# Kernel tuning notes

Measured on AMD Instinct MI355X. Metric: run time of the kernel, lower is better.

## Reference

```python
import math
import jax, jax.numpy as jnp
import numpy as np

B, S, D, N, H = 4, 1024, 1024, 16, 64

def setup_inputs() -> dict:
    key = jax.random.key(0)
    ks = jax.random.split(key, 10)
    sc = 0.02
    return {
        'from_tensor': jax.random.normal(ks[0], (B, S, D), jnp.float32),
        'to_tensor': jax.random.normal(ks[1], (B, S, D), jnp.float32),
        'attention_mask': jnp.ones((B, S, S), jnp.int32),
        'wq': jax.random.normal(ks[2], (D, N, H), jnp.float32) * sc,
        'bq': jnp.zeros((N, H), jnp.float32),
        'wk': jax.random.normal(ks[3], (D, N, H), jnp.float32) * sc,
        'bk': jnp.zeros((N, H), jnp.float32),
        'wv': jax.random.normal(ks[4], (D, N, H), jnp.float32) * sc,
        'bv': jnp.zeros((N, H), jnp.float32),
        'pre_softmax_weight': jax.random.normal(ks[5], (N, N), jnp.float32) * sc,
        'post_softmax_weight': jax.random.normal(ks[6], (N, N), jnp.float32) * sc,
        'wo': jax.random.normal(ks[7], (N, H, D), jnp.float32) * sc,
        'bo': jnp.zeros((D,), jnp.float32),
    }

def reference(from_tensor, to_tensor, attention_mask, wq, bq, wk, bk, wv, bv,
              pre_softmax_weight, post_softmax_weight, wo, bo):
    # QKV projections: [B,S,D] x [D,N,H] -> [B,S,N,H]
    q = jnp.einsum('bfd,dnh->bfnh', from_tensor, wq) + bq
    k = jnp.einsum('btd,dnh->btnh', to_tensor, wk) + bk
    v = jnp.einsum('btd,dnh->btnh', to_tensor, wv) + bv
    # attention scores [B,N,F,T]
    scores = jnp.einsum('btnh,bfnh->bnft', k, q) * (1.0 / math.sqrt(float(H)))
    # pre-softmax head mixing
    scores = jnp.einsum('bnft,nl->blft', scores, pre_softmax_weight)
    # masked softmax (mask expanded at axis 1, additive -10000 on masked)
    mask = attention_mask.astype(scores.dtype)[:, None, :, :]  # [B,1,F,T]
    scores = scores + (1.0 - mask) * -10000.0
    probs = jax.nn.softmax(scores, axis=-1)
    # post-softmax head mixing (dropout rate 0.0 -> identity)
    probs = jnp.einsum('bnft,nl->blft', probs, post_softmax_weight)
    # attend to values and project out
    ctx = jnp.einsum('bnft,btnh->bfnh', probs, v)
    out = jnp.einsum('bfnh,nhd->bfd', ctx, wo) + bo
    return out
```

## Files before the change

kernel.cpp:

```cpp
#include <hip/hip_runtime.h>
#include <hip/hip_bf16.h>

typedef __hip_bfloat16 bf16;
using short8 = __attribute__((ext_vector_type(8))) short;
using f32x4  = __attribute__((ext_vector_type(4))) float;
using f32x2  = __attribute__((ext_vector_type(2))) float;

#ifndef __has_builtin
#define __has_builtin(x) 0
#endif
#if __has_builtin(__builtin_amdgcn_global_load_lds)
#define HAVE_GLL 1
#else
#define HAVE_GLL 0
#endif

__device__ inline void stage16(const short* __restrict__ g, short* l, int lane) {
#if HAVE_GLL
  __builtin_amdgcn_global_load_lds((__attribute__((address_space(1))) void*)g,
                                   (__attribute__((address_space(3))) void*)l,
                                   16, 0, 0);
#else
  *(short8*)(l + lane * 8) = *(const short8*)g;
#endif
}

__device__ inline unsigned pack2bf(float a, float b) {
  bf16 h0 = __float2bfloat16(a), h1 = __float2bfloat16(b);
  return (unsigned)*(unsigned short*)&h0 | ((unsigned)*(unsigned short*)&h1 << 16);
}

__global__ __launch_bounds__(256) void gemm_lds64(
    const bf16* __restrict__ Ag, long a_bs1, long a_bs2, int lda,
    const bf16* __restrict__ Bg, long b_bs1, long b_bs2, int ldb,
    void* __restrict__ Cg, long c_bs1, long c_bs2, int ldc,
    const float* __restrict__ bias, int K, int Z2, float alpha, int cf32)
{
  __shared__ short As[128 * 64];
  __shared__ short Bs[64 * 64];

  int z = blockIdx.z, z1 = z / Z2, z2 = z - z1 * Z2;
  const short* A = (const short*)(Ag + z1 * a_bs1 + z2 * a_bs2);
  const short* B = (const short*)(Bg + z1 * b_bs1 + z2 * b_bs2);

  int tid = threadIdx.x, lane = tid & 63, w = tid >> 6;
  int wm = w & 1, wn = w >> 1;
  int m0 = blockIdx.x * 128, n0 = blockIdx.y * 64;
  int r = lane & 15, q = lane >> 4;

  int srow = lane >> 3, scol = (lane & 7) * 8;
  const short* Asrc = A + (long)(m0 + w * 32 + srow) * lda + scol;
  const short* Bsrc = B + (long)(n0 + w * 16 + srow) * ldb + scol;
  short* Adst = As + (w * 32) * 64;
  short* Bdst = Bs + (w * 16) * 64;

  f32x4 acc[4][2];
  #pragma unroll
  for (int i = 0; i < 4; ++i)
    #pragma unroll
    for (int j = 0; j < 2; ++j) acc[i][j] = (f32x4){0.f, 0.f, 0.f, 0.f};

  for (int kt = 0; kt < K; kt += 64) {
    #pragma unroll
    for (int i = 0; i < 4; ++i)
      stage16(Asrc + (long)i * 8 * lda + kt, Adst + i * 8 * 64, lane);
    #pragma unroll
    for (int i = 0; i < 2; ++i)
      stage16(Bsrc + (long)i * 8 * ldb + kt, Bdst + i * 8 * 64, lane);
    __syncthreads();
    #pragma unroll
    for (int kk = 0; kk < 64; kk += 32) {
      short8 af[4], bfr[2];
      #pragma unroll
      for (int i = 0; i < 4; ++i)
        af[i] = *(const short8*)&As[(wm * 64 + i * 16 + r) * 64 + kk + q * 8];
      #pragma unroll
      for (int j = 0; j < 2; ++j)
        bfr[j] = *(const short8*)&Bs[(wn * 32 + j * 16 + r) * 64 + kk + q * 8];
      #pragma unroll
      for (int i = 0; i < 4; ++i)
        #pragma unroll
        for (int j = 0; j < 2; ++j)
          acc[i][j] = __builtin_amdgcn_mfma_f32_16x16x32_bf16(af[i], bfr[j], acc[i][j], 0, 0, 0);
    }
    __syncthreads();
  }

  long cb = z1 * c_bs1 + z2 * c_bs2;
  #pragma unroll
  for (int j = 0; j < 2; ++j) {
    int col = n0 + wn * 32 + j * 16 + r;
    float bv = bias ? bias[col] : 0.0f;
    #pragma unroll
    for (int i = 0; i < 4; ++i) {
      int row0 = m0 + wm * 64 + i * 16 + q * 4;
      #pragma unroll
      for (int rr = 0; rr < 4; ++rr) {
        float val = acc[i][j][rr] * alpha + bv;
        long idx = cb + (long)(row0 + rr) * ldc + col;
        if (cf32) ((float*)Cg)[idx] = val;
        else ((bf16*)Cg)[idx] = __float2bfloat16(val);
      }
    }
  }
}

struct QKVArgs {
  const bf16* A[3];
  const bf16* Bw[3];
  bf16* C[3];
  const float* bias[3];
};

__global__ __launch_bounds__(256) void gemm_qkv(QKVArgs args) {
  __shared__ short As[128 * 64];
  __shared__ short Bs[64 * 64];

  int z = blockIdx.z;
  const short* A = (const short*)args.A[z];
  const short* B = (const short*)args.Bw[z];
  bf16* C = args.C[z];
  const float* bias = args.bias[z];

  int tid = threadIdx.x, lane = tid & 63, w = tid >> 6;
  int wm = w & 1, wn = w >> 1;
  int m0 = blockIdx.x * 128, n0 = blockIdx.y * 64;
  int r = lane & 15, q = lane >> 4;

  int srow = lane >> 3, scol = (lane & 7) * 8;
  const short* Asrc = A + (long)(m0 + w * 32 + srow) * 1024 + scol;
  const short* Bsrc = B + (long)(n0 + w * 16 + srow) * 1024 + scol;
  short* Adst = As + (w * 32) * 64;
  short* Bdst = Bs + (w * 16) * 64;

  f32x4 acc[4][2];
  #pragma unroll
  for (int i = 0; i < 4; ++i)
    #pragma unroll
    for (int j = 0; j < 2; ++j) acc[i][j] = (f32x4){0.f, 0.f, 0.f, 0.f};

  for (int kt = 0; kt < 1024; kt += 64) {
    #pragma unroll
    for (int i = 0; i < 4; ++i)
      stage16(Asrc + (long)i * 8 * 1024 + kt, Adst + i * 8 * 64, lane);
    #pragma unroll
    for (int i = 0; i < 2; ++i)
      stage16(Bsrc + (long)i * 8 * 1024 + kt, Bdst + i * 8 * 64, lane);
    __syncthreads();
    #pragma unroll
    for (int kk = 0; kk < 64; kk += 32) {
      short8 af[4], bfr[2];
      #pragma unroll
      for (int i = 0; i < 4; ++i)
        af[i] = *(const short8*)&As[(wm * 64 + i * 16 + r) * 64 + kk + q * 8];
      #pragma unroll
      for (int j = 0; j < 2; ++j)
        bfr[j] = *(const short8*)&Bs[(wn * 32 + j * 16 + r) * 64 + kk + q * 8];
      #pragma unroll
      for (int i = 0; i < 4; ++i)
        #pragma unroll
        for (int j = 0; j < 2; ++j)
          acc[i][j] = __builtin_amdgcn_mfma_f32_16x16x32_bf16(af[i], bfr[j], acc[i][j], 0, 0, 0);
    }
    __syncthreads();
  }

  #pragma unroll
  for (int j = 0; j < 2; ++j) {
    int col = n0 + wn * 32 + j * 16 + r;
    float bv = bias[col];
    #pragma unroll
    for (int i = 0; i < 4; ++i) {
      int row0 = m0 + wm * 64 + i * 16 + q * 4;
      #pragma unroll
      for (int rr = 0; rr < 4; ++rr)
        C[(long)(row0 + rr) * 1024 + col] = __float2bfloat16(acc[i][j][rr] + bv);
    }
  }
}

__global__ __launch_bounds__(256) void gemm_k64(
    const bf16* __restrict__ Ag, long a_bs1, long a_bs2, int lda,
    const bf16* __restrict__ Bg, long b_bs1, long b_bs2, int ldb,
    bf16* __restrict__ Cg, long c_bs1, long c_bs2, int ldc,
    int Z2, float alpha)
{
  int z = blockIdx.z, z1 = z / Z2, z2 = z - z1 * Z2;
  const short* A = (const short*)(Ag + z1 * a_bs1 + z2 * a_bs2);
  const short* B = (const short*)(Bg + z1 * b_bs1 + z2 * b_bs2);
  bf16* C = Cg + z1 * c_bs1 + z2 * c_bs2;

  int tid = threadIdx.x, lane = tid & 63, w = tid >> 6;
  int wm = w & 1, wn = w >> 1;
  int m0 = blockIdx.x * 128 + wm * 64;
  int n0 = blockIdx.y * 128 + wn * 64;
  int r = lane & 15, q = lane >> 4;

  const short* Ar = A + (long)(m0 + r) * lda + q * 8;
  const short* Br = B + (long)(n0 + r) * ldb + q * 8;

  f32x4 acc[4][4];
  #pragma unroll
  for (int i = 0; i < 4; ++i)
    #pragma unroll
    for (int j = 0; j < 4; ++j) acc[i][j] = (f32x4){0.f, 0.f, 0.f, 0.f};

  #pragma unroll
  for (int kk = 0; kk < 64; kk += 32) {
    short8 af[4], bfr[4];
    #pragma unroll
    for (int i = 0; i < 4; ++i) af[i] = *(const short8*)(Ar + (long)i * 16 * lda + kk);
    #pragma unroll
    for (int j = 0; j < 4; ++j) bfr[j] = *(const short8*)(Br + (long)j * 16 * ldb + kk);
    #pragma unroll
    for (int i = 0; i < 4; ++i)
      #pragma unroll
      for (int j = 0; j < 4; ++j)
        acc[i][j] = __builtin_amdgcn_mfma_f32_16x16x32_bf16(af[i], bfr[j], acc[i][j], 0, 0, 0);
  }

  #pragma unroll
  for (int j = 0; j < 4; ++j) {
    int col = n0 + j * 16 + r;
    #pragma unroll
    for (int i = 0; i < 4; ++i) {
      int row0 = m0 + i * 16 + q * 4;
      #pragma unroll
      for (int rr = 0; rr < 4; ++rr)
        C[(long)(row0 + rr) * ldc + col] = __float2bfloat16(acc[i][j][rr] * alpha);
    }
  }
}

__global__ __launch_bounds__(256) void cvt2(
    const float* __restrict__ a, const float* __restrict__ b,
    bf16* __restrict__ oa, bf16* __restrict__ ob)
{
  const float* in = blockIdx.y ? b : a;
  bf16* out = blockIdx.y ? ob : oa;
  int i = (blockIdx.x * 256 + threadIdx.x) * 8;
  float4 v0 = *(const float4*)(in + i);
  float4 v1 = *(const float4*)(in + i + 4);
  uint4 pk;
  pk.x = pack2bf(v0.x, v0.y);
  pk.y = pack2bf(v0.z, v0.w);
  pk.z = pack2bf(v1.x, v1.y);
  pk.w = pack2bf(v1.z, v1.w);
  *(uint4*)(out + i) = pk;
}

struct WT4 { const float* s[4]; bf16* d[4]; };

__global__ __launch_bounds__(256) void wtrans4(WT4 a) {
  __shared__ bf16 tile[64][66];
  int z = blockIdx.z;
  const float* in = a.s[z];
  bf16* out = a.d[z];
  int r0 = blockIdx.x * 64, c0 = blockIdx.y * 64;
  int tx = threadIdx.x & 63, ty = threadIdx.x >> 6;
  #pragma unroll
  for (int i = 0; i < 16; ++i) {
    int rr = i * 4 + ty;
    tile[rr][tx] = __float2bfloat16(in[(long)(r0 + rr) * 1024 + c0 + tx]);
  }
  __syncthreads();
  #pragma unroll
  for (int i = 0; i < 16; ++i) {
    int rr = i * 4 + ty;
    out[(long)(c0 + rr) * 1024 + r0 + tx] = tile[tx][rr];
  }
}

__global__ __launch_bounds__(256) void transpose_bf16(
    const bf16* __restrict__ in, long i_bs1, long i_bs2, int i_rs,
    bf16* __restrict__ out, long o_bs1, long o_bs2, int o_rs, int Z2)
{
  __shared__ bf16 tile[64][66];
  int z = blockIdx.z, z1 = z / Z2, z2 = z - z1 * Z2;
  const bf16* ib = in + z1 * i_bs1 + z2 * i_bs2;
  bf16* ob = out + z1 * o_bs1 + z2 * o_bs2;
  int r0 = blockIdx.x * 64, c0 = blockIdx.y * 64;
  int tx = threadIdx.x & 63, ty = threadIdx.x >> 6;
  #pragma unroll
  for (int i = 0; i < 16; ++i) {
    int rr = i * 4 + ty;
    tile[rr][tx] = ib[(long)(r0 + rr) * i_rs + c0 + tx];
  }
  __syncthreads();
  #pragma unroll
  for (int i = 0; i < 16; ++i) {
    int rr = i * 4 + ty;
    ob[(long)(c0 + rr) * o_rs + r0 + tx] = tile[tx][rr];
  }
}

__global__ __launch_bounds__(256) void mixsoftmax2(
    bf16* __restrict__ sc, long sc_bs, const float* __restrict__ pre,
    const float* __restrict__ post, const int* __restrict__ mask)
{
  __shared__ float wpre[256], wpost[256];
  __shared__ float zbuf[16][256];
  __shared__ float zbuf2[16][16];
  __shared__ float zinv[16];
  int tid = threadIdx.x;
  int f = blockIdx.x, b = blockIdx.y;
  wpre[tid] = pre[tid];
  wpost[tid] = post[tid];
  __syncthreads();

  unsigned short* scb = (unsigned short*)(sc + (long)b * sc_bs) + ((long)f << 10);
  const int* mk = mask + ((long)b << 20) + ((long)f << 10);
  int tg = tid * 4;

  uint2 u[16];
  #pragma unroll
  for (int n = 0; n < 16; ++n)
    u[n] = *(const uint2*)(scb + ((long)n << 20) + tg);
  int4 mm = *(const int4*)(mk + tg);
  float madd0 = (1.0f - (float)mm.x) * -10000.0f;
  float madd1 = (1.0f - (float)mm.y) * -10000.0f;
  float madd2 = (1.0f - (float)mm.z) * -10000.0f;
  float madd3 = (1.0f - (float)mm.w) * -10000.0f;

  f32x2 mA[16], mB[16];
  #pragma unroll
  for (int l = 0; l < 16; ++l) {
    mA[l] = (f32x2){madd0, madd1};
    mB[l] = (f32x2){madd2, madd3};
  }

  #pragma unroll
  for (int n = 0; n < 16; ++n) {
    unsigned lo = u[n].x, hi = u[n].y;
    f32x2 s01 = (f32x2){__uint_as_float((lo & 0xffffu) << 16),
                        __uint_as_float(lo & 0xffff0000u)};
    f32x2 s23 = (f32x2){__uint_as_float((hi & 0xffffu) << 16),
                        __uint_as_float(hi & 0xffff0000u)};
    const float4* wr = (const float4*)&wpre[n * 16];
    #pragma unroll
    for (int g = 0; g < 4; ++g) {
      float4 wv = wr[g];
      mA[g * 4 + 0] += s01 * wv.x;  mB[g * 4 + 0] += s23 * wv.x;
      mA[g * 4 + 1] += s01 * wv.y;  mB[g * 4 + 1] += s23 * wv.y;
      mA[g * 4 + 2] += s01 * wv.z;  mB[g * 4 + 2] += s23 * wv.z;
      mA[g * 4 + 3] += s01 * wv.w;  mB[g * 4 + 3] += s23 * wv.w;
    }
  }

  #pragma unroll
  for (int l = 0; l < 16; ++l) {
    mA[l].x = __expf(mA[l].x);  mA[l].y = __expf(mA[l].y);
    mB[l].x = __expf(mB[l].x);  mB[l].y = __expf(mB[l].y);
    zbuf[l][tid] = (mA[l].x + mA[l].y) + (mB[l].x + mB[l].y);
  }
  __syncthreads();
  {
    int l = tid >> 4, c = tid & 15;
    const float4* zr = (const float4*)&zbuf[l][c * 16];
    float4 a0 = zr[0], a1 = zr[1], a2 = zr[2], a3 = zr[3];
    zbuf2[l][c] = ((a0.x + a0.y) + (a0.z + a0.w)) + ((a1.x + a1.y) + (a1.z + a1.w)) +
                  ((a2.x + a2.y) + (a2.z + a2.w)) + ((a3.x + a3.y) + (a3.z + a3.w));
  }
  __syncthreads();
  if (tid < 16) {
    const float4* zr = (const float4*)&zbuf2[tid][0];
    float4 a0 = zr[0], a1 = zr[1], a2 = zr[2], a3 = zr[3];
    float s = ((a0.x + a0.y) + (a0.z + a0.w)) + ((a1.x + a1.y) + (a1.z + a1.w)) +
              ((a2.x + a2.y) + (a2.z + a2.w)) + ((a3.x + a3.y) + (a3.z + a3.w));
    zinv[tid] = 1.0f / s;
  }
  __syncthreads();

  f32x2 oA[16], oB[16];
  #pragma unroll
  for (int l = 0; l < 16; ++l) {
    oA[l] = (f32x2){0.f, 0.f};
    oB[l] = (f32x2){0.f, 0.f};
  }
  #pragma unroll
  for (int n = 0; n < 16; ++n) {
    float zi = zinv[n];
    f32x2 e01 = mA[n] * zi, e23 = mB[n] * zi;
    const float4* wr = (const float4*)&wpost[n * 16];
    #pragma unroll
    for (int g = 0; g < 4; ++g) {
      float4 wv = wr[g];
      oA[g * 4 + 0] += e01 * wv.x;  oB[g * 4 + 0] += e23 * wv.x;
      oA[g * 4 + 1] += e01 * wv.y;  oB[g * 4 + 1] += e23 * wv.y;
      oA[g * 4 + 2] += e01 * wv.z;  oB[g * 4 + 2] += e23 * wv.z;
      oA[g * 4 + 3] += e01 * wv.w;  oB[g * 4 + 3] += e23 * wv.w;
    }
  }
  #pragma unroll
  for (int l = 0; l < 16; ++l) {
    uint2 st;
    st.x = pack2bf(oA[l].x, oA[l].y);
    st.y = pack2bf(oB[l].x, oB[l].y);
    *(uint2*)(scb + ((long)l << 20) + tg) = st;
  }
}

extern "C" void kernel_launch(void* const* d_in, const int* in_sizes, int n_in,
                              void* d_out, int out_size, void* d_ws, size_t ws_size,
                              hipStream_t stream) {
  const float* from = (const float*)d_in[0];
  const float* to   = (const float*)d_in[1];
  const int*  mask  = (const int*)d_in[2];
  const float* wq = (const float*)d_in[3];
  const float* bq = (const float*)d_in[4];
  const float* wk = (const float*)d_in[5];
  const float* bk = (const float*)d_in[6];
  const float* wv = (const float*)d_in[7];
  const float* bv = (const float*)d_in[8];
  const float* pre  = (const float*)d_in[9];
  const float* post = (const float*)d_in[10];
  const float* wo = (const float*)d_in[11];
  const float* bo = (const float*)d_in[12];
  float* out = (float*)d_out;

  bf16* W = (bf16*)d_ws;
  const long M1 = 1048576;
  bool big = ws_size >= (size_t)(85 * M1) * 2;

  bf16 *Sc, *fromB, *toB, *wqT, *wkT, *wvT, *woT, *Q, *Kp, *V, *Vt, *ctx;
  if (big) {
    Sc = W;                 fromB = W;            toB = W + 4 * M1;
    wqT = W + 8 * M1;       wkT = W + 9 * M1;     wvT = W + 10 * M1;
    woT = W + 64 * M1;      Q = W + 65 * M1;      Kp = W + 69 * M1;
    V = W + 73 * M1;        Vt = W + 77 * M1;     ctx = W + 81 * M1;
  } else {
    Sc = W;                 fromB = W;            toB = W + 4 * M1;
    wqT = W + 8 * M1;       wkT = W + 9 * M1;     wvT = W + 10 * M1;
    woT = W + 16 * M1;      Q = W + 17 * M1;      Kp = W + 21 * M1;
    V = W + 25 * M1;        Vt = W + 29 * M1;     ctx = W + 33 * M1;
  }

  dim3 blk(256);

  cvt2<<<dim3(2048, 2), blk, 0, stream>>>(from, to, fromB, toB);
  WT4 wt;
  wt.s[0] = wq; wt.s[1] = wk; wt.s[2] = wv; wt.s[3] = wo;
  wt.d[0] = wqT; wt.d[1] = wkT; wt.d[2] = wvT; wt.d[3] = woT;
  wtrans4<<<dim3(16, 16, 4), blk, 0, stream>>>(wt);

  QKVArgs qa;
  qa.A[0] = fromB; qa.A[1] = toB; qa.A[2] = toB;
  qa.Bw[0] = wqT;  qa.Bw[1] = wkT; qa.Bw[2] = wvT;
  qa.C[0] = Q;     qa.C[1] = Kp;  qa.C[2] = V;
  qa.bias[0] = bq; qa.bias[1] = bk; qa.bias[2] = bv;
  gemm_qkv<<<dim3(32, 16, 3), blk, 0, stream>>>(qa);

  transpose_bf16<<<dim3(16, 1, 64), blk, 0, stream>>>(V, M1, 64, 1024,
                                                      Vt, M1, 65536, 1024, 16);

  if (big) {
    gemm_k64<<<dim3(8, 8, 64), blk, 0, stream>>>(
        Q, M1, 64, 1024, Kp, M1, 64, 1024, Sc, 16 * M1, M1, 1024, 16, 0.125f);
    mixsoftmax2<<<dim3(1024, 4), blk, 0, stream>>>(Sc, 16 * M1, pre, post, mask);
    gemm_lds64<<<dim3(8, 1, 64), blk, 0, stream>>>(
        Sc, 16 * M1, M1, 1024, Vt, M1, 65536, 1024, ctx, M1, 64, 1024, nullptr,
        1024, 16, 1.0f, 0);
  } else {
    for (int b = 0; b < 4; ++b) {
      gemm_k64<<<dim3(8, 8, 16), blk, 0, stream>>>(
          Q + b * M1, 0, 64, 1024, Kp + b * M1, 0, 64, 1024,
          Sc, 0, M1, 1024, 16, 0.125f);
      mixsoftmax2<<<dim3(1024, 1), blk, 0, stream>>>(Sc, 0, pre, post, mask + b * M1);
      gemm_lds64<<<dim3(8, 1, 16), blk, 0, stream>>>(
          Sc, 0, M1, 1024, Vt + b * M1, 0, 65536, 1024,
          ctx + b * M1, 0, 64, 1024, nullptr, 1024, 16, 1.0f, 0);
    }
  }

  gemm_lds64<<<dim3(32, 16, 1), blk, 0, stream>>>(
      ctx, 0, 0, 1024, woT, 0, 0, 1024, out, 0, 0, 1024, bo, 1024, 1, 1.0f, 1);
}
```

Measured before the change: 347.3 us.

## Use MFMA for softmax head mixing and widen projection GEMM N-tiles

Rewrites the mix-softmax kernel so that the pre- and post-softmax 16x16 head-mixing matmuls run on bf16 MFMA instructions instead of scalar FMAs. Scores are staged through padded LDS and row sums are reduced with wave shuffles. Separately, the QKV and output projection GEMMs move from 64- to 128-wide N tiles, halving their grid and increasing reuse of each A tile. Running the head mixing in bf16 MFMA rounds the mixing weights and the probabilities to bf16, which costs some precision. The larger tiles raise register and LDS use per block.

```diff
diff --git a/kernel.cpp b/kernel.cpp
--- a/kernel.cpp
+++ b/kernel.cpp
@@ -4,7 +4,6 @@
 typedef __hip_bfloat16 bf16;
 using short8 = __attribute__((ext_vector_type(8))) short;
 using f32x4  = __attribute__((ext_vector_type(4))) float;
-using f32x2  = __attribute__((ext_vector_type(2))) float;
 
 #ifndef __has_builtin
 #define __has_builtin(x) 0
@@ -30,14 +29,21 @@
   return (unsigned)*(unsigned short*)&h0 | ((unsigned)*(unsigned short*)&h1 << 16);
 }
 
-__global__ __launch_bounds__(256) void gemm_lds64(
+__device__ inline short bfbits(float v) {
+  bf16 h = __float2bfloat16(v);
+  return *(short*)&h;
+}
+
+template <int BN>
+__global__ __launch_bounds__(256) void gemm_lds(
     const bf16* __restrict__ Ag, long a_bs1, long a_bs2, int lda,
     const bf16* __restrict__ Bg, long b_bs1, long b_bs2, int ldb,
     void* __restrict__ Cg, long c_bs1, long c_bs2, int ldc,
     const float* __restrict__ bias, int K, int Z2, float alpha, int cf32)
 {
+  constexpr int WNT = BN / 32;
   __shared__ short As[128 * 64];
-  __shared__ short Bs[64 * 64];
+  __shared__ short Bs[BN * 64];
 
   int z = blockIdx.z, z1 = z / Z2, z2 = z - z1 * Z2;
   const short* A = (const short*)(Ag + z1 * a_bs1 + z2 * a_bs2);
@@ -45,42 +51,42 @@
 
   int tid = threadIdx.x, lane = tid & 63, w = tid >> 6;
   int wm = w & 1, wn = w >> 1;
-  int m0 = blockIdx.x * 128, n0 = blockIdx.y * 64;
+  int m0 = blockIdx.x * 128, n0 = blockIdx.y * BN;
   int r = lane & 15, q = lane >> 4;
 
   int srow = lane >> 3, scol = (lane & 7) * 8;
   const short* Asrc = A + (long)(m0 + w * 32 + srow) * lda + scol;
-  const short* Bsrc = B + (long)(n0 + w * 16 + srow) * ldb + scol;
+  const short* Bsrc = B + (long)(n0 + w * (BN / 4) + srow) * ldb + scol;
   short* Adst = As + (w * 32) * 64;
-  short* Bdst = Bs + (w * 16) * 64;
-
-  f32x4 acc[4][2];
+  short* Bdst = Bs + (w * (BN / 4)) * 64;
+
+  f32x4 acc[4][WNT];
   #pragma unroll
   for (int i = 0; i < 4; ++i)
     #pragma unroll
-    for (int j = 0; j < 2; ++j) acc[i][j] = (f32x4){0.f, 0.f, 0.f, 0.f};
+    for (int j = 0; j < WNT; ++j) acc[i][j] = (f32x4){0.f, 0.f, 0.f, 0.f};
 
   for (int kt = 0; kt < K; kt += 64) {
     #pragma unroll
     for (int i = 0; i < 4; ++i)
       stage16(Asrc + (long)i * 8 * lda + kt, Adst + i * 8 * 64, lane);
     #pragma unroll
-    for (int i = 0; i < 2; ++i)
+    for (int i = 0; i < BN / 32; ++i)
       stage16(Bsrc + (long)i * 8 * ldb + kt, Bdst + i * 8 * 64, lane);
     __syncthreads();
     #pragma unroll
     for (int kk = 0; kk < 64; kk += 32) {
-      short8 af[4], bfr[2];
+      short8 af[4], bfr[WNT];
       #pragma unroll
       for (int i = 0; i < 4; ++i)
         af[i] = *(const short8*)&As[(wm * 64 + i * 16 + r) * 64 + kk + q * 8];
       #pragma unroll
-      for (int j = 0; j < 2; ++j)
-        bfr[j] = *(const short8*)&Bs[(wn * 32 + j * 16 + r) * 64 + kk + q * 8];
+      for (int j = 0; j < WNT; ++j)
+        bfr[j] = *(const short8*)&Bs[(wn * WNT * 16 + j * 16 + r) * 64 + kk + q * 8];
       #pragma unroll
       for (int i = 0; i < 4; ++i)
         #pragma unroll
-        for (int j = 0; j < 2; ++j)
+        for (int j = 0; j < WNT; ++j)
           acc[i][j] = __builtin_amdgcn_mfma_f32_16x16x32_bf16(af[i], bfr[j], acc[i][j], 0, 0, 0);
     }
     __syncthreads();
@@ -88,8 +94,8 @@
 
   long cb = z1 * c_bs1 + z2 * c_bs2;
   #pragma unroll
-  for (int j = 0; j < 2; ++j) {
-    int col = n0 + wn * 32 + j * 16 + r;
+  for (int j = 0; j < WNT; ++j) {
+    int col = n0 + wn * WNT * 16 + j * 16 + r;
     float bv = bias ? bias[col] : 0.0f;
     #pragma unroll
     for (int i = 0; i < 4; ++i) {
@@ -114,7 +120,7 @@
 
 __global__ __launch_bounds__(256) void gemm_qkv(QKVArgs args) {
   __shared__ short As[128 * 64];
-  __shared__ short Bs[64 * 64];
+  __shared__ short Bs[128 * 64];
 
   int z = blockIdx.z;
   const short* A = (const short*)args.A[z];
@@ -124,50 +130,50 @@
 
   int tid = threadIdx.x, lane = tid & 63, w = tid >> 6;
   int wm = w & 1, wn = w >> 1;
-  int m0 = blockIdx.x * 128, n0 = blockIdx.y * 64;
+  int m0 = blockIdx.x * 128, n0 = blockIdx.y * 128;
   int r = lane & 15, q = lane >> 4;
 
   int srow = lane >> 3, scol = (lane & 7) * 8;
   const short* Asrc = A + (long)(m0 + w * 32 + srow) * 1024 + scol;
-  const short* Bsrc = B + (long)(n0 + w * 16 + srow) * 1024 + scol;
+  const short* Bsrc = B + (long)(n0 + w * 32 + srow) * 1024 + scol;
   short* Adst = As + (w * 32) * 64;
-  short* Bdst = Bs + (w * 16) * 64;
-
-  f32x4 acc[4][2];
+  short* Bdst = Bs + (w * 32) * 64;
+
+  f32x4 acc[4][4];
   #pragma unroll
   for (int i = 0; i < 4; ++i)
     #pragma unroll
-    for (int j = 0; j < 2; ++j) acc[i][j] = (f32x4){0.f, 0.f, 0.f, 0.f};
+    for (int j = 0; j < 4; ++j) acc[i][j] = (f32x4){0.f, 0.f, 0.f, 0.f};
 
   for (int kt = 0; kt < 1024; kt += 64) {
     #pragma unroll
     for (int i = 0; i < 4; ++i)
       stage16(Asrc + (long)i * 8 * 1024 + kt, Adst + i * 8 * 64, lane);
     #pragma unroll
-    for (int i = 0; i < 2; ++i)
+    for (int i = 0; i < 4; ++i)
       stage16(Bsrc + (long)i * 8 * 1024 + kt, Bdst + i * 8 * 64, lane);
     __syncthreads();
     #pragma unroll
     for (int kk = 0; kk < 64; kk += 32) {
-      short8 af[4], bfr[2];
+      short8 af[4], bfr[4];
       #pragma unroll
       for (int i = 0; i < 4; ++i)
         af[i] = *(const short8*)&As[(wm * 64 + i * 16 + r) * 64 + kk + q * 8];
       #pragma unroll
-      for (int j = 0; j < 2; ++j)
-        bfr[j] = *(const short8*)&Bs[(wn * 32 + j * 16 + r) * 64 + kk + q * 8];
+      for (int j = 0; j < 4; ++j)
+        bfr[j] = *(const short8*)&Bs[(wn * 64 + j * 16 + r) * 64 + kk + q * 8];
       #pragma unroll
       for (int i = 0; i < 4; ++i)
         #pragma unroll
-        for (int j = 0; j < 2; ++j)
+        for (int j = 0; j < 4; ++j)
           acc[i][j] = __builtin_amdgcn_mfma_f32_16x16x32_bf16(af[i], bfr[j], acc[i][j], 0, 0, 0);
     }
     __syncthreads();
   }
 
   #pragma unroll
-  for (int j = 0; j < 2; ++j) {
-    int col = n0 + wn * 32 + j * 16 + r;
+  for (int j = 0; j < 4; ++j) {
+    int col = n0 + wn * 64 + j * 16 + r;
     float bv = bias[col];
     #pragma unroll
     for (int i = 0; i < 4; ++i) {
@@ -294,109 +300,99 @@
   }
 }
 
-__global__ __launch_bounds__(256) void mixsoftmax2(
+#define SST 1028
+
+__global__ __launch_bounds__(256) void mixsoftmax3(
     bf16* __restrict__ sc, long sc_bs, const float* __restrict__ pre,
     const float* __restrict__ post, const int* __restrict__ mask)
 {
-  __shared__ float wpre[256], wpost[256];
-  __shared__ float zbuf[16][256];
-  __shared__ float zbuf2[16][16];
-  __shared__ float zinv[16];
-  int tid = threadIdx.x;
+  __shared__ short scs[16 * SST];
+  __shared__ float zpart[4][16];
+  __shared__ float zinvs[16];
+
+  int tid = threadIdx.x, lane = tid & 63, w = tid >> 6;
+  int q = lane >> 4, r = lane & 15, qq = q & 1;
   int f = blockIdx.x, b = blockIdx.y;
-  wpre[tid] = pre[tid];
-  wpost[tid] = post[tid];
+
+  short* scb = (short*)(sc + (long)b * sc_bs) + ((long)f << 10);
+  const int* mk = mask + ((long)b << 20) + ((long)f << 10);
+
+  #pragma unroll
+  for (int i = 0; i < 16; ++i) {
+    int s = i * 256 + tid;
+    int n = s >> 8, off = (s & 255) * 4;
+    *(uint2*)&scs[n * SST + off] = *(const uint2*)(scb + ((long)n << 20) + off);
+  }
+
+  short8 a1 = {}, a2 = {};
+  #pragma unroll
+  for (int j = 0; j < 8; ++j) {
+    int n = q * 8 + j;
+    float v1 = (q < 2) ? pre[(n & 15) * 16 + r] : 0.0f;
+    float v2 = (q < 2) ? post[(n & 15) * 16 + r] : 0.0f;
+    a1[j] = bfbits(v1);
+    a2[j] = bfbits(v2);
+  }
   __syncthreads();
 
-  unsigned short* scb = (unsigned short*)(sc + (long)b * sc_bs) + ((long)f << 10);
-  const int* mk = mask + ((long)b << 20) + ((long)f << 10);
-  int tg = tid * 4;
-
-  uint2 u[16];
-  #pragma unroll
-  for (int n = 0; n < 16; ++n)
-    u[n] = *(const uint2*)(scb + ((long)n << 20) + tg);
-  int4 mm = *(const int4*)(mk + tg);
-  float madd0 = (1.0f - (float)mm.x) * -10000.0f;
-  float madd1 = (1.0f - (float)mm.y) * -10000.0f;
-  float madd2 = (1.0f - (float)mm.z) * -10000.0f;
-  float madd3 = (1.0f - (float)mm.w) * -10000.0f;
-
-  f32x2 mA[16], mB[16];
-  #pragma unroll
-  for (int l = 0; l < 16; ++l) {
-    mA[l] = (f32x2){madd0, madd1};
-    mB[l] = (f32x2){madd2, madd3};
-  }
-
-  #pragma unroll
-  for (int n = 0; n < 16; ++n) {
-    unsigned lo = u[n].x, hi = u[n].y;
-    f32x2 s01 = (f32x2){__uint_as_float((lo & 0xffffu) << 16),
-                        __uint_as_float(lo & 0xffff0000u)};
-    f32x2 s23 = (f32x2){__uint_as_float((hi & 0xffffu) << 16),
-                        __uint_as_float(hi & 0xffff0000u)};
-    const float4* wr = (const float4*)&wpre[n * 16];
+  int wt0 = w * 256;
+  float E[16][4];
+  float zl[4] = {0.f, 0.f, 0.f, 0.f};
+
+  #pragma unroll
+  for (int s = 0; s < 16; ++s) {
+    int t0 = wt0 + s * 16;
+    short8 b1;
+    #pragma unroll
+    for (int j = 0; j < 8; ++j)
+      b1[j] = scs[(qq * 8 + j) * SST + t0 + r];
+    float madd = (1.0f - (float)mk[t0 + r]) * -10000.0f;
+    f32x4 c = {madd, madd, madd, madd};
+    f32x4 d = __builtin_amdgcn_mfma_f32_16x16x32_bf16(a1, b1, c, 0, 0, 0);
     #pragma unroll
     for (int g = 0; g < 4; ++g) {
-      float4 wv = wr[g];
-      mA[g * 4 + 0] += s01 * wv.x;  mB[g * 4 + 0] += s23 * wv.x;
-      mA[g * 4 + 1] += s01 * wv.y;  mB[g * 4 + 1] += s23 * wv.y;
-      mA[g * 4 + 2] += s01 * wv.z;  mB[g * 4 + 2] += s23 * wv.z;
-      mA[g * 4 + 3] += s01 * wv.w;  mB[g * 4 + 3] += s23 * wv.w;
-    }
-  }
-
-  #pragma unroll
-  for (int l = 0; l < 16; ++l) {
-    mA[l].x = __expf(mA[l].x);  mA[l].y = __expf(mA[l].y);
-    mB[l].x = __expf(mB[l].x);  mB[l].y = __expf(mB[l].y);
-    zbuf[l][tid] = (mA[l].x + mA[l].y) + (mB[l].x + mB[l].y);
-  }
+      float e = __expf(d[g]);
+      E[s][g] = e;
+      zl[g] += e;
+    }
+  }
+
+  #pragma unroll
+  for (int off = 8; off >= 1; off >>= 1)
+    #pragma unroll
+    for (int g = 0; g < 4; ++g)
+      zl[g] += __shfl_down(zl[g], off);
+  if (r == 0)
+    #pragma unroll
+    for (int g = 0; g < 4; ++g)
+      zpart[w][q * 4 + g] = zl[g];
   __syncthreads();
-  {
-    int l = tid >> 4, c = tid & 15;
-    const float4* zr = (const float4*)&zbuf[l][c * 16];
-    float4 a0 = zr[0], a1 = zr[1], a2 = zr[2], a3 = zr[3];
-    zbuf2[l][c] = ((a0.x + a0.y) + (a0.z + a0.w)) + ((a1.x + a1.y) + (a1.z + a1.w)) +
-                  ((a2.x + a2.y) + (a2.z + a2.w)) + ((a3.x + a3.y) + (a3.z + a3.w));
-  }
+  if (tid < 16)
+    zinvs[tid] = 1.0f / (zpart[0][tid] + zpart[1][tid] + zpart[2][tid] + zpart[3][tid]);
   __syncthreads();
-  if (tid < 16) {
-    const float4* zr = (const float4*)&zbuf2[tid][0];
-    float4 a0 = zr[0], a1 = zr[1], a2 = zr[2], a3 = zr[3];
-    float s = ((a0.x + a0.y) + (a0.z + a0.w)) + ((a1.x + a1.y) + (a1.z + a1.w)) +
-              ((a2.x + a2.y) + (a2.z + a2.w)) + ((a3.x + a3.y) + (a3.z + a3.w));
-    zinv[tid] = 1.0f / s;
-  }
-  __syncthreads();
-
-  f32x2 oA[16], oB[16];
-  #pragma unroll
-  for (int l = 0; l < 16; ++l) {
-    oA[l] = (f32x2){0.f, 0.f};
-    oB[l] = (f32x2){0.f, 0.f};
-  }
-  #pragma unroll
-  for (int n = 0; n < 16; ++n) {
-    float zi = zinv[n];
-    f32x2 e01 = mA[n] * zi, e23 = mB[n] * zi;
-    const float4* wr = (const float4*)&wpost[n * 16];
-    #pragma unroll
-    for (int g = 0; g < 4; ++g) {
-      float4 wv = wr[g];
-      oA[g * 4 + 0] += e01 * wv.x;  oB[g * 4 + 0] += e23 * wv.x;
-      oA[g * 4 + 1] += e01 * wv.y;  oB[g * 4 + 1] += e23 * wv.y;
-      oA[g * 4 + 2] += e01 * wv.z;  oB[g * 4 + 2] += e23 * wv.z;
-      oA[g * 4 + 3] += e01 * wv.w;  oB[g * 4 + 3] += e23 * wv.w;
-    }
-  }
-  #pragma unroll
-  for (int l = 0; l < 16; ++l) {
-    uint2 st;
-    st.x = pack2bf(oA[l].x, oA[l].y);
-    st.y = pack2bf(oB[l].x, oB[l].y);
-    *(uint2*)(scb + ((long)l << 20) + tg) = st;
+
+  float zi[4];
+  #pragma unroll
+  for (int g = 0; g < 4; ++g) zi[g] = zinvs[q * 4 + g];
+
+  #pragma unroll
+  for (int s = 0; s < 16; ++s) {
+    int t0 = wt0 + s * 16;
+    float pe[4];
+    #pragma unroll
+    for (int g = 0; g < 4; ++g) pe[g] = E[s][g] * zi[g];
+    short8 b2;
+    #pragma unroll
+    for (int j = 0; j < 8; ++j) {
+      int n = qq * 8 + j;
+      float v = __shfl(pe[n & 3], ((n >> 2) << 4) + r);
+      b2[j] = bfbits(v);
+    }
+    f32x4 zero = {0.f, 0.f, 0.f, 0.f};
+    f32x4 p = __builtin_amdgcn_mfma_f32_16x16x32_bf16(a2, b2, zero, 0, 0, 0);
+    #pragma unroll
+    for (int g = 0; g < 4; ++g)
+      scb[((long)(q * 4 + g) << 20) + t0 + r] = bfbits(p[g]);
   }
 }
 
@@ -448,7 +444,7 @@
   qa.Bw[0] = wqT;  qa.Bw[1] = wkT; qa.Bw[2] = wvT;
   qa.C[0] = Q;     qa.C[1] = Kp;  qa.C[2] = V;
   qa.bias[0] = bq; qa.bias[1] = bk; qa.bias[2] = bv;
-  gemm_qkv<<<dim3(32, 16, 3), blk, 0, stream>>>(qa);
+  gemm_qkv<<<dim3(32, 8, 3), blk, 0, stream>>>(qa);
 
   transpose_bf16<<<dim3(16, 1, 64), blk, 0, stream>>>(V, M1, 64, 1024,
                                                       Vt, M1, 65536, 1024, 16);
@@ -456,8 +452,8 @@
   if (big) {
     gemm_k64<<<dim3(8, 8, 64), blk, 0, stream>>>(
         Q, M1, 64, 1024, Kp, M1, 64, 1024, Sc, 16 * M1, M1, 1024, 16, 0.125f);
-    mixsoftmax2<<<dim3(1024, 4), blk, 0, stream>>>(Sc, 16 * M1, pre, post, mask);
-    gemm_lds64<<<dim3(8, 1, 64), blk, 0, stream>>>(
+    mixsoftmax3<<<dim3(1024, 4), blk, 0, stream>>>(Sc, 16 * M1, pre, post, mask);
+    gemm_lds<64><<<dim3(8, 1, 64), blk, 0, stream>>>(
         Sc, 16 * M1, M1, 1024, Vt, M1, 65536, 1024, ctx, M1, 64, 1024, nullptr,
         1024, 16, 1.0f, 0);
   } else {
@@ -465,13 +461,13 @@
       gemm_k64<<<dim3(8, 8, 16), blk, 0, stream>>>(
           Q + b * M1, 0, 64, 1024, Kp + b * M1, 0, 64, 1024,
           Sc, 0, M1, 1024, 16, 0.125f);
-      mixsoftmax2<<<dim3(1024, 1), blk, 0, stream>>>(Sc, 0, pre, post, mask + b * M1);
-      gemm_lds64<<<dim3(8, 1, 16), blk, 0, stream>>>(
+      mixsoftmax3<<<dim3(1024, 1), blk, 0, stream>>>(Sc, 0, pre, post, mask + b * M1);
+      gemm_lds<64><<<dim3(8, 1, 16), blk, 0, stream>>>(
           Sc, 0, M1, 1024, Vt + b * M1, 0, 65536, 1024,
           ctx + b * M1, 0, 64, 1024, nullptr, 1024, 16, 1.0f, 0);
     }
   }
 
-  gemm_lds64<<<dim3(32, 16, 1), blk, 0, stream>>>(
+  gemm_lds<128><<<dim3(32, 8, 1), blk, 0, stream>>>(
       ctx, 0, 0, 1024, woT, 0, 0, 1024, out, 0, 0, 1024, bo, 1024, 1, 1.0f, 1);
 }
```

After: 382.0 us. 1.1x slower.
